# Performance work log

Hardware: AMD Instinct MI355X
Metric: run time of the kernel (lower is better)

Reference implementation:

```python
import jax, jax.numpy as jnp
import numpy as np

H = 32      # num_attention_heads
HD = 64     # head_dim
MD = 64     # qk_mqa_dim (rope dim)
EPS = 1e-6
SCALING = (HD + MD) ** -0.5
NEG = -1e9


def rms_norm(x, w):
    var = jnp.mean(jnp.square(x), axis=-1, keepdims=True)
    return x * jax.lax.rsqrt(var + EPS) * w


def rotate_half(x):
    x1, x2 = jnp.split(x, 2, axis=-1)
    return jnp.concatenate([-x2, x1], axis=-1)


def apply_rope(x, cos, sin):
    return x * cos + rotate_half(x) * sin


def setup_inputs() -> dict:
    key = jax.random.key(0)
    ks = jax.random.split(key, 6)
    B, S, D = 1, 2048, 2048
    QR, KVR = 1024, 896
    hidden_states = jax.random.normal(ks[0], (B, S, D), jnp.float32)
    # real rotary tables for the MD-dim rope subspace
    inv_freq = 1.0 / (10000.0 ** (np.arange(0, MD, 2, dtype=np.float32) / MD))
    freqs = np.arange(S, dtype=np.float32)[:, None] * inv_freq[None, :]
    emb = np.concatenate([freqs, freqs], axis=-1)  # [S, MD]
    cos = jnp.asarray(np.cos(emb), jnp.float32)
    sin = jnp.asarray(np.sin(emb), jnp.float32)
    s = 0.02
    Wqa = jax.random.normal(ks[1], (QR, D), jnp.float32) * s
    q_ln_w = jnp.ones((QR,), jnp.float32)
    Wqb = jax.random.normal(ks[2], (H * (HD + MD), QR), jnp.float32) * s
    Wkva = jax.random.normal(ks[3], (KVR + MD, D), jnp.float32) * s
    kv_ln_w = jnp.ones((KVR,), jnp.float32)
    Wkvb = jax.random.normal(ks[4], (2 * H * HD, KVR), jnp.float32) * s
    Wo = jax.random.normal(ks[5], (D, H * HD), jnp.float32) * s
    return {"hidden_states": hidden_states, "cos": cos, "sin": sin,
            "Wqa": Wqa, "q_ln_w": q_ln_w, "Wqb": Wqb,
            "Wkva": Wkva, "kv_ln_w": kv_ln_w, "Wkvb": Wkvb, "Wo": Wo}


def reference(hidden_states, cos, sin, Wqa, q_ln_w, Wqb, Wkva, kv_ln_w, Wkvb, Wo):
    B, S, D = hidden_states.shape
    KVR = kv_ln_w.shape[0]
    # Q: LoRA down -> RMSNorm -> up (weights pre-absorbed with rope split)
    q = rms_norm(hidden_states @ Wqa.T, q_ln_w) @ Wqb.T      # [B,S,H*(HD+MD)]
    q = q.reshape(B, S, H, HD + MD).transpose(0, 2, 1, 3)     # [B,H,S,HD+MD]
    q_nope, q_rope = q[..., :HD], q[..., HD:]
    # KV: shared compressed latent + MQA rope key
    ckv = hidden_states @ Wkva.T                               # [B,S,KVR+MD]
    kv_nope, k_rope = ckv[..., :KVR], ckv[..., KVR:]
    kv_nope = rms_norm(kv_nope, kv_ln_w)
    q_rope = apply_rope(q_rope, cos[None, None], sin[None, None])
    k_rope = apply_rope(k_rope[:, None], cos[None, None], sin[None, None])  # [B,1,S,MD]
    # up-project latent to per-head K_nope and V (interleaved per head)
    kv = (kv_nope @ Wkvb.T).reshape(B, S, H, 2 * HD).transpose(0, 2, 1, 3)  # [B,H,S,2*HD]
    k_nope, value = kv[..., :HD], kv[..., HD:]
    key_states = jnp.concatenate(
        [k_nope, jnp.broadcast_to(k_rope, (B, H, S, MD))], axis=-1)  # repeat_kv of rope part
    query_states = jnp.concatenate([q_nope, q_rope], axis=-1)        # [B,H,S,HD+MD]
    # causal SDPA with scaling = (head_dim + qk_mqa_dim)^-0.5
    scores = jnp.einsum('bhqd,bhkd->bhqk', query_states, key_states) * SCALING
    causal = jnp.tril(jnp.ones((S, S), bool))
    scores = jnp.where(causal[None, None], scores, NEG)
    probs = jax.nn.softmax(scores, axis=-1)
    out = jnp.einsum('bhqk,bhkd->bhqd', probs, value)                # [B,H,S,HD]
    out = out.transpose(0, 2, 1, 3).reshape(B, S, H * HD)
    return out @ Wo.T
```

## Files before the change

kernel.cpp:

```cpp
#include <hip/hip_runtime.h>
#include <stdint.h>

typedef unsigned short u16;
typedef __attribute__((ext_vector_type(4))) float f32x4;
typedef __attribute__((ext_vector_type(4))) unsigned short u16x4;
typedef __attribute__((ext_vector_type(8))) unsigned short u16x8;
typedef __attribute__((ext_vector_type(8))) short s16x8;
typedef __attribute__((ext_vector_type(4))) short s16x4;
typedef __attribute__((ext_vector_type(2))) unsigned int u32x2;

#define DEVI static __device__ __forceinline__

DEVI u16 f2b(float f) {
  union { float f; unsigned u; } v; v.f = f;
  unsigned r = v.u + 0x7fffu + ((v.u >> 16) & 1u);
  return (u16)(r >> 16);
}
DEVI float b2f(u16 b) {
  union { unsigned u; float f; } v; v.u = ((unsigned)b) << 16;
  return v.f;
}

DEVI void gload_lds16(const void* gptr, void* lptr) {
  typedef const __attribute__((address_space(1))) unsigned gq;
  typedef __attribute__((address_space(3))) unsigned lq;
  __builtin_amdgcn_global_load_lds((gq*)(uintptr_t)gptr,
                                   (lq*)(uint32_t)(uintptr_t)lptr, 16, 0, 0);
}

DEVI unsigned cvtpk(float a, float b) {
  unsigned d;
  asm("v_cvt_pk_bf16_f32 %0, %1, %2" : "=v"(d) : "v"(a), "v"(b));
  return d;
}
DEVI f32x4 mfma16(s16x4 a, s16x4 b, f32x4 c) {
  f32x4 d;
  asm("v_mfma_f32_16x16x16_bf16 %0, %1, %2, %3" : "=v"(d) : "v"(a), "v"(b), "v"(c));
  return d;
}
DEVI float exp2a(float x) {
  float d;
  asm("v_exp_f32 %0, %1" : "=v"(d) : "v"(x));
  return d;
}

__global__ __launch_bounds__(256) void cvt_all(
    const float* __restrict__ X, const float* __restrict__ Wqa,
    const float* __restrict__ Wkva, const float* __restrict__ Wqb,
    const float* __restrict__ Wkvb, const float* __restrict__ Wo,
    u16* __restrict__ Xb, u16* __restrict__ W1, u16* __restrict__ Wqbb,
    u16* __restrict__ Wkvbb, u16* __restrict__ Wob) {
  int i = blockIdx.x * 256 + threadIdx.x;
  const int stride = gridDim.x * 256;
  for (; i < 5079040; i += stride) {
    const float* s; u16* d; int j;
    if (i < 1572864) {
      if (i < 1048576) { s = X; d = Xb; j = i; }
      else             { s = Wqa; d = W1; j = i - 1048576; }
    } else if (i < 3112960) {
      if (i < 2064384) { s = Wkva; d = W1 + 1024 * 2048; j = i - 1572864; }
      else             { s = Wqb; d = Wqbb; j = i - 2064384; }
    } else {
      if (i < 4030464) { s = Wkvb; d = Wkvbb; j = i - 3112960; }
      else             { s = Wo; d = Wob; j = i - 4030464; }
    }
    f32x4 v = *(const f32x4*)(s + (size_t)j * 4);
    u16x4 o;
    o[0] = f2b(v[0]); o[1] = f2b(v[1]); o[2] = f2b(v[2]); o[3] = f2b(v[3]);
    *(u16x4*)(d + (size_t)j * 4) = o;
  }
}

#define GEMM_STAGE(AP, BP, KK, k0, buf)                                        \
  {                                                                            \
    _Pragma("unroll") for (int p = 0; p < 4; ++p) {                            \
      const int c = tid + p * 256;                                             \
      const int row = c >> 3, j = c & 7;                                       \
      gload_lds16(AP + (size_t)(m0 + row) * (KK) + (k0) + ((j ^ (row & 7)) * 8), \
                  &As[buf][c * 8]);                                            \
    }                                                                          \
    _Pragma("unroll") for (int p = 0; p < 4; ++p) {                            \
      const int c = tid + p * 256;                                             \
      const int row = c >> 3, j = c & 7;                                       \
      gload_lds16(BP + (size_t)(n0 + row) * (KK) + (k0) + ((j ^ (row & 7)) * 8), \
                  &Bs[buf][c * 8]);                                            \
    }                                                                          \
  }

#define GEMM_COMPUTE(cur)                                                      \
  _Pragma("unroll") for (int kk = 0; kk < 64; kk += 32) {                      \
    s16x8 af[4], bfr[4];                                                       \
    _Pragma("unroll") for (int i = 0; i < 4; ++i) {                            \
      const int rA = wm * 64 + i * 16 + c15;                                   \
      af[i] = *(const s16x8*)((const char*)&As[cur][0] + rA * 128 +            \
                              (((kk + g * 8) * 2) ^ ((rA & 7) << 4)));         \
    }                                                                          \
    _Pragma("unroll") for (int i = 0; i < 4; ++i) {                            \
      const int rB = wn * 64 + i * 16 + c15;                                   \
      bfr[i] = *(const s16x8*)((const char*)&Bs[cur][0] + rB * 128 +           \
                               (((kk + g * 8) * 2) ^ ((rB & 7) << 4)));        \
    }                                                                          \
    _Pragma("unroll") for (int i = 0; i < 4; ++i)                              \
      _Pragma("unroll") for (int j = 0; j < 4; ++j)                            \
        acc[i][j] = __builtin_amdgcn_mfma_f32_16x16x32_bf16(af[i], bfr[j],     \
                                                            acc[i][j], 0, 0, 0); \
  }

#define GEMM_PROLOG                                                            \
  const int tid = threadIdx.x;                                                 \
  const int lane = tid & 63, w = tid >> 6;                                     \
  const int wm = w >> 1, wn = w & 1;                                           \
  const int c15 = lane & 15, g = lane >> 4;                                    \
  const int m0 = blockIdx.y * 128, n0 = blockIdx.x * 128;                      \
  f32x4 acc[4][4] = {};

#define GEMM_LOOP(AP, BP, KK)                                                  \
  GEMM_STAGE(AP, BP, KK, 0, 0);                                                \
  __syncthreads();                                                             \
  const int nk = (KK) >> 6;                                                    \
  for (int kt = 0; kt < nk; ++kt) {                                            \
    const int cur = kt & 1;                                                    \
    if (kt + 1 < nk) GEMM_STAGE(AP, BP, KK, (kt + 1) << 6, cur ^ 1);           \
    GEMM_COMPUTE(cur);                                                         \
    __syncthreads();                                                           \
  }

__global__ __launch_bounds__(256) void gemm_f32(const u16* __restrict__ A,
                                                const u16* __restrict__ B,
                                                float* __restrict__ C,
                                                int M, int N, int K) {
  __shared__ __align__(16) u16 As[2][128 * 64];
  __shared__ __align__(16) u16 Bs[2][128 * 64];
  GEMM_PROLOG
  GEMM_LOOP(A, B, K)
#pragma unroll
  for (int i = 0; i < 4; ++i)
#pragma unroll
    for (int j = 0; j < 4; ++j) {
      const int mr = m0 + wm * 64 + i * 16 + g * 4;
      const int nc = n0 + wn * 64 + j * 16 + c15;
#pragma unroll
      for (int r = 0; r < 4; ++r)
        C[(size_t)(mr + r) * N + nc] = acc[i][j][r];
    }
}

__global__ __launch_bounds__(256) void gemm2_fused(
    const u16* __restrict__ qn, const u16* __restrict__ Wqbb,
    const u16* __restrict__ kvn, const u16* __restrict__ Wkvbb,
    u16* __restrict__ qraw, char* __restrict__ KbB, char* __restrict__ VtB) {
  __shared__ __align__(16) u16 As[2][128 * 64];
  __shared__ __align__(16) u16 Bs[2][128 * 64];
  const int z = blockIdx.z;
  const u16* A = z ? kvn : qn;
  const u16* B = z ? Wkvbb : Wqbb;
  const int K = z ? 896 : 1024;
  GEMM_PROLOG
  GEMM_LOOP(A, B, K)

  if (z == 0) {
#pragma unroll
    for (int i = 0; i < 4; ++i)
#pragma unroll
      for (int j = 0; j < 4; ++j) {
        const int mr = m0 + wm * 64 + i * 16 + g * 4;
        const int nc = n0 + wn * 64 + j * 16 + c15;
#pragma unroll
        for (int r = 0; r < 4; ++r)
          qraw[(size_t)(mr + r) * 4096 + nc] = f2b(acc[i][j][r]);
      }
  } else {
    const int h = n0 >> 7;
#pragma unroll
    for (int i = 0; i < 4; ++i)
#pragma unroll
      for (int j = 0; j < 4; ++j) {
        const int mr = m0 + wm * 64 + i * 16 + g * 4;
        if (wn == 0) {
          const int d = j * 16 + c15;
#pragma unroll
          for (int r = 0; r < 4; ++r) {
            const int s = mr + r;
            *(u16*)(KbB + ((size_t)(h * 2048 + s) << 8) +
                    ((2 * d) ^ ((s & 7) << 4))) = f2b(acc[i][j][r]);
          }
        } else {
          const int d = j * 16 + c15;
          u16x4 o;
#pragma unroll
          for (int r = 0; r < 4; ++r) o[r] = f2b(acc[i][j][r]);
          *(u16x4*)(VtB + ((size_t)(h * 64 + d) << 12) +
                    ((2 * mr) ^ ((d & 7) << 4))) = o;
        }
      }
  }
}

DEVI float block_sum(float v, float* sbuf, int tid) {
#pragma unroll
  for (int o = 32; o; o >>= 1) v += __shfl_xor(v, o, 64);
  __syncthreads();
  if ((tid & 63) == 0) sbuf[tid >> 6] = v;
  __syncthreads();
  return sbuf[0] + sbuf[1] + sbuf[2] + sbuf[3];
}

__global__ __launch_bounds__(256) void norm_rope(const float* __restrict__ C1,
    const float* __restrict__ qw, const float* __restrict__ kw,
    const float* __restrict__ cosb, const float* __restrict__ sinb,
    u16* __restrict__ qn, u16* __restrict__ kvn, char* __restrict__ KbB) {
  __shared__ float sbuf[4];
  __shared__ __align__(16) u16 rv[64];
  const int s = blockIdx.x, tid = threadIdx.x;
  const float* row = C1 + (size_t)s * 2048;

  f32x4 qv = *(const f32x4*)(row + tid * 4);
  float ss = qv[0]*qv[0] + qv[1]*qv[1] + qv[2]*qv[2] + qv[3]*qv[3];
  ss = block_sum(ss, sbuf, tid);
  const float scale = rsqrtf(ss * (1.f / 1024.f) + 1e-6f);
  {
    f32x4 wv = *(const f32x4*)(qw + tid * 4);
    u16x4 o;
#pragma unroll
    for (int j = 0; j < 4; ++j) o[j] = f2b(qv[j] * scale * wv[j]);
    *(u16x4*)(qn + (size_t)s * 1024 + tid * 4) = o;
  }

  float ss2 = 0.f;
  f32x4 kvv = {};
  if (tid < 224) {
    kvv = *(const f32x4*)(row + 1024 + tid * 4);
    ss2 = kvv[0]*kvv[0] + kvv[1]*kvv[1] + kvv[2]*kvv[2] + kvv[3]*kvv[3];
  }
  ss2 = block_sum(ss2, sbuf, tid);
  const float sc2 = rsqrtf(ss2 * (1.f / 896.f) + 1e-6f);
  if (tid < 224) {
    f32x4 wv = *(const f32x4*)(kw + tid * 4);
    u16x4 o;
#pragma unroll
    for (int j = 0; j < 4; ++j) o[j] = f2b(kvv[j] * sc2 * wv[j]);
    *(u16x4*)(kvn + (size_t)s * 896 + tid * 4) = o;
  }

  if (tid < 64) {
    const int d = tid;
    const float x = row[1920 + d];
    const float part = row[1920 + (d < 32 ? d + 32 : d - 32)];
    const float cv = cosb[s * 64 + d], sv = sinb[s * 64 + d];
    rv[d] = f2b(d < 32 ? (x * cv - part * sv) : (x * cv + part * sv));
  }
  __syncthreads();
  {
    const int h = tid >> 3, c8 = tid & 7;
    const u16x8 v = *(const u16x8*)&rv[c8 * 8];
    *(u16x8*)(KbB + ((size_t)(h * 2048 + s) << 8) +
              ((128 + c8 * 16) ^ ((s & 7) << 4))) = v;
  }
}

__global__ __launch_bounds__(256) void attn_fwd(
    const u16* __restrict__ Qb, const u16* __restrict__ Kb,
    const u16* __restrict__ Vt, const float* __restrict__ cosb,
    const float* __restrict__ sinb, u16* __restrict__ attn) {
  __shared__ __align__(16) u16 Klds[2][64 * 128];
  __shared__ __align__(16) u16 Vlds[2][64 * 64];
  const int tid = threadIdx.x;
  const int lane = tid & 63, w = tid >> 6;
  const int c15 = lane & 15, g = lane >> 4;
  const int orig = blockIdx.x;
  const int l = (orig & 7) * 128 + (orig >> 3);
  const int h = l >> 5;
  const int qb = 31 - (l & 31);
  const int qrow = qb * 64 + w * 16 + c15;
  const char* KbHB = (const char*)Kb + ((size_t)h << 19);
  const char* VtHB = (const char*)Vt + ((size_t)h << 18);
  const float SC2 = 0.12753860478587782f;

  s16x8 qf[4];
  {
    const u16* qp = Qb + (size_t)qrow * 4096 + h * 128;
    u16x8 x0 = *(const u16x8*)(qp + g * 8);
    u16x8 x1 = *(const u16x8*)(qp + 32 + g * 8);
    u16x8 x2 = *(const u16x8*)(qp + 64 + g * 8);
    u16x8 x3 = *(const u16x8*)(qp + 96 + g * 8);
    const float* cb = cosb + (size_t)qrow * 64 + g * 8;
    const float* sb = sinb + (size_t)qrow * 64 + g * 8;
#pragma unroll
    for (int i = 0; i < 8; ++i) {
      qf[0][i] = (short)f2b(b2f(x0[i]) * SC2);
      qf[1][i] = (short)f2b(b2f(x1[i]) * SC2);
      const float f2 = b2f(x2[i]), f3 = b2f(x3[i]);
      qf[2][i] = (short)f2b((f2 * cb[i] - f3 * sb[i]) * SC2);
      qf[3][i] = (short)f2b((f3 * cb[32 + i] + f2 * sb[32 + i]) * SC2);
    }
  }

  const int nt = qb + 1;
  auto STAGE = [&](int t, int buf) {
    const int kv0 = t << 6;
#pragma unroll
    for (int p = 0; p < 4; ++p) {
      const int c = tid + p * 256;
      gload_lds16(KbHB + ((size_t)(kv0 + (c >> 4)) << 8) + (c & 15) * 16,
                  (char*)Klds[buf] + c * 16);
    }
#pragma unroll
    for (int p = 0; p < 2; ++p) {
      const int c = tid + p * 256;
      gload_lds16(VtHB + ((size_t)(c >> 3) << 12) + 2 * kv0 + (c & 7) * 16,
                  (char*)Vlds[buf] + c * 16);
    }
  };

  f32x4 acc[4] = {};
  float m = -1e9f, ssum = 0.f;

  STAGE(0, 0);
  __syncthreads();

  for (int t = 0; t < nt; ++t) {
    const int cur = t & 1;
    const int kv0 = t << 6;
    if (t + 1 < nt) STAGE(t + 1, cur ^ 1);

    const u16* Kc = Klds[cur];
    const u16* Vc = Vlds[cur];

    float pv[4][4];
    float pm = -1e9f;
    __builtin_amdgcn_s_setprio(1);
#pragma unroll
    for (int kvh = 0; kvh < 4; ++kvh) {
      f32x4 s4 = {};
      const int rb = (kvh * 16 + c15) * 256;
#pragma unroll
      for (int d0 = 0; d0 < 4; ++d0) {
        s16x8 kf = *(const s16x8*)((const char*)Kc + rb +
                                   ((d0 * 64 + g * 16) ^ ((c15 & 7) << 4)));
        s4 = __builtin_amdgcn_mfma_f32_16x16x32_bf16(kf, qf[d0], s4, 0, 0, 0);
      }
      pv[kvh][0] = s4[0]; pv[kvh][1] = s4[1];
      pv[kvh][2] = s4[2]; pv[kvh][3] = s4[3];
    }
    __builtin_amdgcn_s_setprio(0);
    if (t == nt - 1) {
#pragma unroll
      for (int kvh = 0; kvh < 4; ++kvh)
#pragma unroll
        for (int r = 0; r < 4; ++r) {
          const int kv = kv0 + kvh * 16 + g * 4 + r;
          if (kv > qrow) pv[kvh][r] = -1e9f;
        }
    }
#pragma unroll
    for (int kvh = 0; kvh < 4; ++kvh)
#pragma unroll
      for (int r = 0; r < 4; ++r) pm = fmaxf(pm, pv[kvh][r]);
    pm = fmaxf(pm, __shfl_xor(pm, 16, 64));
    pm = fmaxf(pm, __shfl_xor(pm, 32, 64));
    if (!__all(pm - m <= 8.f)) {
      const float mnew = fmaxf(m, pm);
      const float alpha = exp2a(m - mnew);
      ssum *= alpha;
#pragma unroll
      for (int dt = 0; dt < 4; ++dt) acc[dt] *= alpha;
      m = mnew;
    }
#pragma unroll
    for (int kvh = 0; kvh < 4; ++kvh)
#pragma unroll
      for (int r = 0; r < 4; ++r) {
        const float p = exp2a(pv[kvh][r] - m);
        pv[kvh][r] = p;
        ssum += p;
      }

    s16x4 pB[4];
#pragma unroll
    for (int ks = 0; ks < 4; ++ks) {
      u32x2 pw;
      pw[0] = cvtpk(pv[ks][0], pv[ks][1]);
      pw[1] = cvtpk(pv[ks][2], pv[ks][3]);
      pB[ks] = __builtin_bit_cast(s16x4, pw);
    }
    __builtin_amdgcn_s_setprio(1);
#pragma unroll
    for (int dt = 0; dt < 4; ++dt) {
      const int rb2 = (dt * 16 + c15) * 128;
#pragma unroll
      for (int ks = 0; ks < 4; ++ks) {
        s16x4 vf = *(const s16x4*)((const char*)Vc + rb2 +
                                   ((ks * 32 + g * 8) ^ ((c15 & 7) << 4)));
        acc[dt] = mfma16(vf, pB[ks], acc[dt]);
      }
    }
    __builtin_amdgcn_s_setprio(0);
    __syncthreads();
  }

  ssum += __shfl_xor(ssum, 16, 64);
  ssum += __shfl_xor(ssum, 32, 64);
  const float inv = 1.f / ssum;
#pragma unroll
  for (int dt = 0; dt < 4; ++dt) {
    u16x4 o;
#pragma unroll
    for (int r = 0; r < 4; ++r) o[r] = f2b(acc[dt][r] * inv);
    *(u16x4*)(attn + (size_t)qrow * 2048 + h * 64 + dt * 16 + g * 4) = o;
  }
}

extern "C" void kernel_launch(void* const* d_in, const int* in_sizes, int n_in,
                              void* d_out, int out_size, void* d_ws, size_t ws_size,
                              hipStream_t stream) {
  const float* X    = (const float*)d_in[0];
  const float* cosb = (const float*)d_in[1];
  const float* sinb = (const float*)d_in[2];
  const float* Wqa  = (const float*)d_in[3];
  const float* qlnw = (const float*)d_in[4];
  const float* Wqb  = (const float*)d_in[5];
  const float* Wkva = (const float*)d_in[6];
  const float* klnw = (const float*)d_in[7];
  const float* Wkvb = (const float*)d_in[8];
  const float* Wo   = (const float*)d_in[9];
  float* out = (float*)d_out;
  char* ws = (char*)d_ws;

  u16*   Xb     = (u16*)(ws + 0);
  u16*   W1     = (u16*)(ws + 8388608);
  float* C1     = (float*)(ws + 16777216);
  u16*   qn     = (u16*)(ws + 33554432);
  u16*   kvn    = (u16*)(ws + 37748736);
  u16*   Wqbb   = (u16*)(ws + 41943040);
  u16*   Wkvbb  = (u16*)(ws + 50331648);
  u16*   qraw_b = (u16*)(ws + 0);
  u16*   Kb     = (u16*)(ws + 58720256);
  u16*   VtG    = (u16*)(ws + 75497472);
  u16*   attnb  = (u16*)(ws + 83886080);
  u16*   Wob    = (u16*)(ws + 92274688);

  cvt_all<<<2048, 256, 0, stream>>>(X, Wqa, Wkva, Wqb, Wkvb, Wo,
                                    Xb, W1, Wqbb, Wkvbb, Wob);

  gemm_f32<<<dim3(16, 16), 256, 0, stream>>>(Xb, W1, C1, 2048, 2048, 2048);

  norm_rope<<<2048, 256, 0, stream>>>(C1, qlnw, klnw, cosb, sinb, qn, kvn, (char*)Kb);

  gemm2_fused<<<dim3(32, 16, 2), 256, 0, stream>>>(qn, Wqbb, kvn, Wkvbb,
                                                   qraw_b, (char*)Kb, (char*)VtG);

  attn_fwd<<<1024, 256, 0, stream>>>(qraw_b, Kb, VtG, cosb, sinb, attnb);

  gemm_f32<<<dim3(16, 16), 256, 0, stream>>>(attnb, Wob, out, 2048, 2048, 2048);
}
```

Baseline: 190.5 us.

## Process 128 query rows per attention block and store first GEMM output as bf16

```diff
diff --git a/kernel.cpp b/kernel.cpp
--- a/kernel.cpp
+++ b/kernel.cpp
@@ -125,9 +125,10 @@
     __syncthreads();                                                           \
   }
 
-__global__ __launch_bounds__(256) void gemm_f32(const u16* __restrict__ A,
+template <int OUT_BF16>
+__global__ __launch_bounds__(256) void gemm_out(const u16* __restrict__ A,
                                                 const u16* __restrict__ B,
-                                                float* __restrict__ C,
+                                                void* __restrict__ Cv,
                                                 int M, int N, int K) {
   __shared__ __align__(16) u16 As[2][128 * 64];
   __shared__ __align__(16) u16 Bs[2][128 * 64];
@@ -140,8 +141,12 @@
       const int mr = m0 + wm * 64 + i * 16 + g * 4;
       const int nc = n0 + wn * 64 + j * 16 + c15;
 #pragma unroll
-      for (int r = 0; r < 4; ++r)
-        C[(size_t)(mr + r) * N + nc] = acc[i][j][r];
+      for (int r = 0; r < 4; ++r) {
+        if (OUT_BF16)
+          ((u16*)Cv)[(size_t)(mr + r) * N + nc] = f2b(acc[i][j][r]);
+        else
+          ((float*)Cv)[(size_t)(mr + r) * N + nc] = acc[i][j][r];
+      }
     }
 }
 
@@ -205,47 +210,49 @@
   return sbuf[0] + sbuf[1] + sbuf[2] + sbuf[3];
 }
 
-__global__ __launch_bounds__(256) void norm_rope(const float* __restrict__ C1,
+__global__ __launch_bounds__(256) void norm_rope(const u16* __restrict__ C1b,
     const float* __restrict__ qw, const float* __restrict__ kw,
     const float* __restrict__ cosb, const float* __restrict__ sinb,
     u16* __restrict__ qn, u16* __restrict__ kvn, char* __restrict__ KbB) {
   __shared__ float sbuf[4];
   __shared__ __align__(16) u16 rv[64];
   const int s = blockIdx.x, tid = threadIdx.x;
-  const float* row = C1 + (size_t)s * 2048;
-
-  f32x4 qv = *(const f32x4*)(row + tid * 4);
-  float ss = qv[0]*qv[0] + qv[1]*qv[1] + qv[2]*qv[2] + qv[3]*qv[3];
+  const u16* row = C1b + (size_t)s * 2048;
+
+  u16x4 qv4 = *(const u16x4*)(row + tid * 4);
+  float q0 = b2f(qv4[0]), q1 = b2f(qv4[1]), q2 = b2f(qv4[2]), q3 = b2f(qv4[3]);
+  float ss = q0*q0 + q1*q1 + q2*q2 + q3*q3;
   ss = block_sum(ss, sbuf, tid);
   const float scale = rsqrtf(ss * (1.f / 1024.f) + 1e-6f);
   {
     f32x4 wv = *(const f32x4*)(qw + tid * 4);
     u16x4 o;
-#pragma unroll
-    for (int j = 0; j < 4; ++j) o[j] = f2b(qv[j] * scale * wv[j]);
+    o[0] = f2b(q0 * scale * wv[0]); o[1] = f2b(q1 * scale * wv[1]);
+    o[2] = f2b(q2 * scale * wv[2]); o[3] = f2b(q3 * scale * wv[3]);
     *(u16x4*)(qn + (size_t)s * 1024 + tid * 4) = o;
   }
 
   float ss2 = 0.f;
-  f32x4 kvv = {};
+  float k0 = 0, k1 = 0, k2 = 0, k3 = 0;
   if (tid < 224) {
-    kvv = *(const f32x4*)(row + 1024 + tid * 4);
-    ss2 = kvv[0]*kvv[0] + kvv[1]*kvv[1] + kvv[2]*kvv[2] + kvv[3]*kvv[3];
+    u16x4 kv4 = *(const u16x4*)(row + 1024 + tid * 4);
+    k0 = b2f(kv4[0]); k1 = b2f(kv4[1]); k2 = b2f(kv4[2]); k3 = b2f(kv4[3]);
+    ss2 = k0*k0 + k1*k1 + k2*k2 + k3*k3;
   }
   ss2 = block_sum(ss2, sbuf, tid);
   const float sc2 = rsqrtf(ss2 * (1.f / 896.f) + 1e-6f);
   if (tid < 224) {
     f32x4 wv = *(const f32x4*)(kw + tid * 4);
     u16x4 o;
-#pragma unroll
-    for (int j = 0; j < 4; ++j) o[j] = f2b(kvv[j] * sc2 * wv[j]);
+    o[0] = f2b(k0 * sc2 * wv[0]); o[1] = f2b(k1 * sc2 * wv[1]);
+    o[2] = f2b(k2 * sc2 * wv[2]); o[3] = f2b(k3 * sc2 * wv[3]);
     *(u16x4*)(kvn + (size_t)s * 896 + tid * 4) = o;
   }
 
   if (tid < 64) {
     const int d = tid;
-    const float x = row[1920 + d];
-    const float part = row[1920 + (d < 32 ? d + 32 : d - 32)];
+    const float x = b2f(row[1920 + d]);
+    const float part = b2f(row[1920 + (d < 32 ? d + 32 : d - 32)]);
     const float cv = cosb[s * 64 + d], sv = sinb[s * 64 + d];
     rv[d] = f2b(d < 32 ? (x * cv - part * sv) : (x * cv + part * sv));
   }
@@ -268,16 +275,19 @@
   const int lane = tid & 63, w = tid >> 6;
   const int c15 = lane & 15, g = lane >> 4;
   const int orig = blockIdx.x;
-  const int l = (orig & 7) * 128 + (orig >> 3);
-  const int h = l >> 5;
-  const int qb = 31 - (l & 31);
-  const int qrow = qb * 64 + w * 16 + c15;
+  const int xcd = orig & 7, l = orig >> 3;
+  const int h = xcd * 4 + (l & 3);
+  const int qb = 15 - (l >> 2);
+  const int wmin = qb * 128 + w * 32;
+  const int wmax = wmin + 31;
   const char* KbHB = (const char*)Kb + ((size_t)h << 19);
   const char* VtHB = (const char*)Vt + ((size_t)h << 18);
   const float SC2 = 0.12753860478587782f;
 
-  s16x8 qf[4];
-  {
+  s16x8 qf[2][4];
+#pragma unroll
+  for (int qa = 0; qa < 2; ++qa) {
+    const int qrow = wmin + qa * 16 + c15;
     const u16* qp = Qb + (size_t)qrow * 4096 + h * 128;
     u16x8 x0 = *(const u16x8*)(qp + g * 8);
     u16x8 x1 = *(const u16x8*)(qp + 32 + g * 8);
@@ -287,15 +297,15 @@
     const float* sb = sinb + (size_t)qrow * 64 + g * 8;
 #pragma unroll
     for (int i = 0; i < 8; ++i) {
-      qf[0][i] = (short)f2b(b2f(x0[i]) * SC2);
-      qf[1][i] = (short)f2b(b2f(x1[i]) * SC2);
+      qf[qa][0][i] = (short)f2b(b2f(x0[i]) * SC2);
+      qf[qa][1][i] = (short)f2b(b2f(x1[i]) * SC2);
       const float f2 = b2f(x2[i]), f3 = b2f(x3[i]);
-      qf[2][i] = (short)f2b((f2 * cb[i] - f3 * sb[i]) * SC2);
-      qf[3][i] = (short)f2b((f3 * cb[32 + i] + f2 * sb[32 + i]) * SC2);
-    }
-  }
-
-  const int nt = qb + 1;
+      qf[qa][2][i] = (short)f2b((f2 * cb[i] - f3 * sb[i]) * SC2);
+      qf[qa][3][i] = (short)f2b((f3 * cb[32 + i] + f2 * sb[32 + i]) * SC2);
+    }
+  }
+
+  const int nt = 2 * qb + 2;
   auto STAGE = [&](int t, int buf) {
     const int kv0 = t << 6;
 #pragma unroll
@@ -312,8 +322,8 @@
     }
   };
 
-  f32x4 acc[4] = {};
-  float m = -1e9f, ssum = 0.f;
+  f32x4 acc[2][4] = {};
+  float m[2] = {-1e9f, -1e9f}, ssum[2] = {0.f, 0.f};
 
   STAGE(0, 0);
   __syncthreads();
@@ -323,90 +333,112 @@
     const int kv0 = t << 6;
     if (t + 1 < nt) STAGE(t + 1, cur ^ 1);
 
-    const u16* Kc = Klds[cur];
-    const u16* Vc = Vlds[cur];
-
-    float pv[4][4];
-    float pm = -1e9f;
-    __builtin_amdgcn_s_setprio(1);
-#pragma unroll
-    for (int kvh = 0; kvh < 4; ++kvh) {
-      f32x4 s4 = {};
-      const int rb = (kvh * 16 + c15) * 256;
-#pragma unroll
-      for (int d0 = 0; d0 < 4; ++d0) {
-        s16x8 kf = *(const s16x8*)((const char*)Kc + rb +
+    if (kv0 <= wmax) {
+      const u16* Kc = Klds[cur];
+      const u16* Vc = Vlds[cur];
+
+      float pv[2][4][4];
+      __builtin_amdgcn_s_setprio(1);
+#pragma unroll
+      for (int kvh = 0; kvh < 4; ++kvh) {
+        s16x8 kf[4];
+        const int rb = (kvh * 16 + c15) * 256;
+#pragma unroll
+        for (int d0 = 0; d0 < 4; ++d0)
+          kf[d0] = *(const s16x8*)((const char*)Kc + rb +
                                    ((d0 * 64 + g * 16) ^ ((c15 & 7) << 4)));
-        s4 = __builtin_amdgcn_mfma_f32_16x16x32_bf16(kf, qf[d0], s4, 0, 0, 0);
-      }
-      pv[kvh][0] = s4[0]; pv[kvh][1] = s4[1];
-      pv[kvh][2] = s4[2]; pv[kvh][3] = s4[3];
-    }
-    __builtin_amdgcn_s_setprio(0);
-    if (t == nt - 1) {
-#pragma unroll
-      for (int kvh = 0; kvh < 4; ++kvh)
-#pragma unroll
-        for (int r = 0; r < 4; ++r) {
-          const int kv = kv0 + kvh * 16 + g * 4 + r;
-          if (kv > qrow) pv[kvh][r] = -1e9f;
-        }
-    }
-#pragma unroll
-    for (int kvh = 0; kvh < 4; ++kvh)
-#pragma unroll
-      for (int r = 0; r < 4; ++r) pm = fmaxf(pm, pv[kvh][r]);
-    pm = fmaxf(pm, __shfl_xor(pm, 16, 64));
-    pm = fmaxf(pm, __shfl_xor(pm, 32, 64));
-    if (!__all(pm - m <= 8.f)) {
-      const float mnew = fmaxf(m, pm);
-      const float alpha = exp2a(m - mnew);
-      ssum *= alpha;
-#pragma unroll
-      for (int dt = 0; dt < 4; ++dt) acc[dt] *= alpha;
-      m = mnew;
-    }
-#pragma unroll
-    for (int kvh = 0; kvh < 4; ++kvh)
-#pragma unroll
-      for (int r = 0; r < 4; ++r) {
-        const float p = exp2a(pv[kvh][r] - m);
-        pv[kvh][r] = p;
-        ssum += p;
-      }
-
-    s16x4 pB[4];
-#pragma unroll
-    for (int ks = 0; ks < 4; ++ks) {
-      u32x2 pw;
-      pw[0] = cvtpk(pv[ks][0], pv[ks][1]);
-      pw[1] = cvtpk(pv[ks][2], pv[ks][3]);
-      pB[ks] = __builtin_bit_cast(s16x4, pw);
-    }
-    __builtin_amdgcn_s_setprio(1);
+#pragma unroll
+        for (int qa = 0; qa < 2; ++qa) {
+          f32x4 s4 = {};
+#pragma unroll
+          for (int d0 = 0; d0 < 4; ++d0)
+            s4 = __builtin_amdgcn_mfma_f32_16x16x32_bf16(kf[d0], qf[qa][d0], s4, 0, 0, 0);
+          pv[qa][kvh][0] = s4[0]; pv[qa][kvh][1] = s4[1];
+          pv[qa][kvh][2] = s4[2]; pv[qa][kvh][3] = s4[3];
+        }
+      }
+      __builtin_amdgcn_s_setprio(0);
+
+      if (kv0 + 63 > wmin) {
+#pragma unroll
+        for (int qa = 0; qa < 2; ++qa) {
+          const int qrow = wmin + qa * 16 + c15;
+#pragma unroll
+          for (int kvh = 0; kvh < 4; ++kvh)
+#pragma unroll
+            for (int r = 0; r < 4; ++r) {
+              const int kv = kv0 + kvh * 16 + g * 4 + r;
+              if (kv > qrow) pv[qa][kvh][r] = -1e9f;
+            }
+        }
+      }
+
+      s16x4 pB[2][4];
+#pragma unroll
+      for (int qa = 0; qa < 2; ++qa) {
+        float pm = -1e9f;
+#pragma unroll
+        for (int kvh = 0; kvh < 4; ++kvh)
+#pragma unroll
+          for (int r = 0; r < 4; ++r) pm = fmaxf(pm, pv[qa][kvh][r]);
+        pm = fmaxf(pm, __shfl_xor(pm, 16, 64));
+        pm = fmaxf(pm, __shfl_xor(pm, 32, 64));
+        if (!__all(pm - m[qa] <= 8.f)) {
+          const float mnew = fmaxf(m[qa], pm);
+          const float alpha = exp2a(m[qa] - mnew);
+          ssum[qa] *= alpha;
+#pragma unroll
+          for (int dt = 0; dt < 4; ++dt) acc[qa][dt] *= alpha;
+          m[qa] = mnew;
+        }
+#pragma unroll
+        for (int kvh = 0; kvh < 4; ++kvh)
+#pragma unroll
+          for (int r = 0; r < 4; ++r) {
+            const float p = exp2a(pv[qa][kvh][r] - m[qa]);
+            pv[qa][kvh][r] = p;
+            ssum[qa] += p;
+          }
+#pragma unroll
+        for (int ks = 0; ks < 4; ++ks) {
+          u32x2 pw;
+          pw[0] = cvtpk(pv[qa][ks][0], pv[qa][ks][1]);
+          pw[1] = cvtpk(pv[qa][ks][2], pv[qa][ks][3]);
+          pB[qa][ks] = __builtin_bit_cast(s16x4, pw);
+        }
+      }
+
+      __builtin_amdgcn_s_setprio(1);
+#pragma unroll
+      for (int dt = 0; dt < 4; ++dt) {
+        const int rb2 = (dt * 16 + c15) * 128;
+#pragma unroll
+        for (int ks = 0; ks < 4; ++ks) {
+          s16x4 vf = *(const s16x4*)((const char*)Vc + rb2 +
+                                     ((ks * 32 + g * 8) ^ ((c15 & 7) << 4)));
+          acc[0][dt] = mfma16(vf, pB[0][ks], acc[0][dt]);
+          acc[1][dt] = mfma16(vf, pB[1][ks], acc[1][dt]);
+        }
+      }
+      __builtin_amdgcn_s_setprio(0);
+    }
+    __syncthreads();
+  }
+
+#pragma unroll
+  for (int qa = 0; qa < 2; ++qa) {
+    float sv = ssum[qa];
+    sv += __shfl_xor(sv, 16, 64);
+    sv += __shfl_xor(sv, 32, 64);
+    const float inv = 1.f / sv;
+    const int qrow = wmin + qa * 16 + c15;
 #pragma unroll
     for (int dt = 0; dt < 4; ++dt) {
-      const int rb2 = (dt * 16 + c15) * 128;
-#pragma unroll
-      for (int ks = 0; ks < 4; ++ks) {
-        s16x4 vf = *(const s16x4*)((const char*)Vc + rb2 +
-                                   ((ks * 32 + g * 8) ^ ((c15 & 7) << 4)));
-        acc[dt] = mfma16(vf, pB[ks], acc[dt]);
-      }
-    }
-    __builtin_amdgcn_s_setprio(0);
-    __syncthreads();
-  }
-
-  ssum += __shfl_xor(ssum, 16, 64);
-  ssum += __shfl_xor(ssum, 32, 64);
-  const float inv = 1.f / ssum;
-#pragma unroll
-  for (int dt = 0; dt < 4; ++dt) {
-    u16x4 o;
-#pragma unroll
-    for (int r = 0; r < 4; ++r) o[r] = f2b(acc[dt][r] * inv);
-    *(u16x4*)(attn + (size_t)qrow * 2048 + h * 64 + dt * 16 + g * 4) = o;
+      u16x4 o;
+#pragma unroll
+      for (int r = 0; r < 4; ++r) o[r] = f2b(acc[qa][dt][r] * inv);
+      *(u16x4*)(attn + (size_t)qrow * 2048 + h * 64 + dt * 16 + g * 4) = o;
+    }
   }
 }
 
@@ -428,7 +460,7 @@
 
   u16*   Xb     = (u16*)(ws + 0);
   u16*   W1     = (u16*)(ws + 8388608);
-  float* C1     = (float*)(ws + 16777216);
+  u16*   C1b    = (u16*)(ws + 16777216);
   u16*   qn     = (u16*)(ws + 33554432);
   u16*   kvn    = (u16*)(ws + 37748736);
   u16*   Wqbb   = (u16*)(ws + 41943040);
@@ -442,14 +474,14 @@
   cvt_all<<<2048, 256, 0, stream>>>(X, Wqa, Wkva, Wqb, Wkvb, Wo,
                                     Xb, W1, Wqbb, Wkvbb, Wob);
 
-  gemm_f32<<<dim3(16, 16), 256, 0, stream>>>(Xb, W1, C1, 2048, 2048, 2048);
-
-  norm_rope<<<2048, 256, 0, stream>>>(C1, qlnw, klnw, cosb, sinb, qn, kvn, (char*)Kb);
+  gemm_out<1><<<dim3(16, 16), 256, 0, stream>>>(Xb, W1, C1b, 2048, 2048, 2048);
+
+  norm_rope<<<2048, 256, 0, stream>>>(C1b, qlnw, klnw, cosb, sinb, qn, kvn, (char*)Kb);
 
   gemm2_fused<<<dim3(32, 16, 2), 256, 0, stream>>>(qn, Wqbb, kvn, Wkvbb,
                                                    qraw_b, (char*)Kb, (char*)VtG);
 
-  attn_fwd<<<1024, 256, 0, stream>>>(qraw_b, Kb, VtG, cosb, sinb, attnb);
-
-  gemm_f32<<<dim3(16, 16), 256, 0, stream>>>(attnb, Wob, out, 2048, 2048, 2048);
-}
+  attn_fwd<<<512, 256, 0, stream>>>(qraw_b, Kb, VtG, cosb, sinb, attnb);
+
+  gemm_out<0><<<dim3(16, 16), 256, 0, stream>>>(attnb, Wob, out, 2048, 2048, 2048);
+}
```

Measured after the change: 182.8 us. 4.1% less time.
